# Optimization experiments

Measured on AMD Instinct MI355X. Metric: run time of the kernel, lower is better.

The kernel has to match this reference:

```python
import jax, jax.numpy as jnp
import numpy as np

V, D, H, B, T = 32000, 256, 512, 32, 64


def setup_inputs() -> dict:
    key = jax.random.key(0)
    ks = jax.random.split(key, 8)
    return {
        "word_indices": jax.random.randint(ks[0], (B, T), 0, V),
        "num_words": jax.random.randint(ks[1], (B,), 1, T + 1),
        "encoder_state": jax.random.normal(ks[2], (B, H), jnp.float32),
        # learned params
        "embW": jax.random.uniform(ks[3], (V, D), jnp.float32, -1.0, 1.0),
        "Wg": jax.random.normal(ks[4], (D + H, 2 * H), jnp.float32) * 0.05,  # reset+update gates
        "bg": jnp.ones((2 * H,), jnp.float32),  # TF GRUCell gate bias init = 1.0
        "Wc": jax.random.normal(ks[5], (D + H, H), jnp.float32) * 0.05,      # candidate
        "bc": jnp.zeros((H,), jnp.float32),
        "Wout": jax.random.normal(ks[6], (H, V), jnp.float32) * 0.05,        # Dense(V)
        "bout": jnp.zeros((V,), jnp.float32),
    }


def reference(word_indices, num_words, encoder_state, embW, Wg, bg, Wc, bc, Wout, bout):
    # Embedding lookup: [B, T, D] -> time-major [T, B, D]
    xs = jnp.swapaxes(embW[word_indices], 0, 1)
    # sequence-length mask like tf.nn.static_rnn: [T, B, 1]
    mask = (jnp.arange(T)[:, None] < num_words[None, :])[..., None].astype(xs.dtype)

    def step(h, inp):
        x_t, m_t = inp  # [B, D], [B, 1]
        xh = jnp.concatenate([x_t, h], axis=-1)          # [B, D+H]
        r, u = jnp.split(jax.nn.sigmoid(xh @ Wg + bg), 2, axis=-1)
        c = jnp.tanh(jnp.concatenate([x_t, r * h], axis=-1) @ Wc + bc)
        h_new = u * h + (1.0 - u) * c
        out = h_new * m_t                                 # zero outputs past seq length
        h_next = m_t * h_new + (1.0 - m_t) * h            # carry state past seq length
        return h_next, out

    _, outs = jax.lax.scan(step, encoder_state, (xs, mask))  # outs: [T, B, H]
    logits = jnp.einsum('tbh,hv->btv', outs, Wout) + bout    # [B, T, V]
    return logits
```

## Files before the change

kernel.cpp:

```cpp
#include <hip/hip_runtime.h>
#include <hip/hip_bf16.h>

#define V_ 32000
#define D_ 256
#define H_ 512
#define B_ 32
#define T_ 64
#define NSL 8

typedef __attribute__((ext_vector_type(8))) __bf16 bf16x8;
typedef __attribute__((ext_vector_type(4))) float f32x4;
typedef _Float16 f16x2 __attribute__((ext_vector_type(2)));
typedef unsigned int u32t;
typedef unsigned short u16t;
typedef unsigned long long u64t;

__device__ __forceinline__ u32t pack_h16(float a, float b) {
  union { _Float16 h; unsigned short u; } lo, hi;
  lo.h = (_Float16)a; hi.h = (_Float16)b;
  return (u32t)lo.u | ((u32t)hi.u << 16);
}

__device__ __forceinline__ float f16u_to_f(u16t u) {
  union { _Float16 h; unsigned short u; } x;
  x.u = u;
  return (float)x.h;
}

__device__ __forceinline__ float dot2(u32t w, u32t h, float acc) {
#if __has_builtin(__builtin_amdgcn_fdot2)
  return __builtin_amdgcn_fdot2(__builtin_bit_cast(f16x2, w),
                                __builtin_bit_cast(f16x2, h), acc, false);
#else
  f16x2 a = __builtin_bit_cast(f16x2, w);
  f16x2 b = __builtin_bit_cast(f16x2, h);
  return acc + (float)a.x * (float)b.x + (float)a.y * (float)b.y;
#endif
}

__device__ __forceinline__ void gld_lds16(const void* g, void* l) {
  __builtin_amdgcn_global_load_lds((const __attribute__((address_space(1))) void*)g,
                                   (__attribute__((address_space(3))) void*)l,
                                   16, 0, 0);
}

__device__ __forceinline__ u32t ld_rlx(const u32t* p) {
  return __hip_atomic_load(p, __ATOMIC_RELAXED, __HIP_MEMORY_SCOPE_AGENT);
}
__device__ __forceinline__ void st_rlx(u32t* p, u32t v) {
  __hip_atomic_store(p, v, __ATOMIC_RELAXED, __HIP_MEMORY_SCOPE_AGENT);
}

__global__ __launch_bounds__(256) void k_setup(const float* __restrict__ Wout,
                                               __hip_bfloat16* __restrict__ WoutT,
                                               const float* __restrict__ Wg,
                                               const float* __restrict__ Wc,
                                               const float* __restrict__ enc,
                                               uint4* __restrict__ Wg2,
                                               uint4* __restrict__ Wc2,
                                               u32t* __restrict__ HBT,
                                               u32t* __restrict__ RHT,
                                               const int* __restrict__ widx,
                                               const float* __restrict__ embW,
                                               const float* __restrict__ bg,
                                               const float* __restrict__ bc,
                                               float* __restrict__ pre_g,
                                               float* __restrict__ pre_c) {
  int blk = blockIdx.x;
  int tid = threadIdx.x;

  if (blk < 4000) {
    __shared__ float tile[64][65];
    int v0 = (blk % 500) * 64;
    int h0 = (blk / 500) * 64;
#pragma unroll
    for (int i = 0; i < 16; ++i) {
      int idx = i * 256 + tid;
      int r = idx >> 6;
      int c = idx & 63;
      tile[r][c] = Wout[(size_t)(h0 + r) * V_ + v0 + c];
    }
    __syncthreads();
#pragma unroll
    for (int i = 0; i < 16; ++i) {
      int idx = i * 256 + tid;
      int rv = idx >> 6;
      int ch = idx & 63;
      WoutT[(size_t)(v0 + rv) * H_ + h0 + ch] = __float2bfloat16(tile[ch][rv]);
    }
  } else if (blk < 4448) {
    int pblk = blk - 4000;
    if (pblk < 256) {
      int gid = pblk * 256 + tid;
      int ks = gid & 3;
      int cq = (gid >> 2) & 127;
      int it = (gid >> 9) & 15;
      int s = gid >> 13;
      int j = (cq < 64) ? (s * 64 + cq) : (512 + s * 64 + (cq - 64));
      int k0 = ks * 128 + it * 8;
      uint4 v;
      v.x = pack_h16(Wg[(size_t)(256 + k0 + 0) * 1024 + j], Wg[(size_t)(256 + k0 + 1) * 1024 + j]);
      v.y = pack_h16(Wg[(size_t)(256 + k0 + 2) * 1024 + j], Wg[(size_t)(256 + k0 + 3) * 1024 + j]);
      v.z = pack_h16(Wg[(size_t)(256 + k0 + 4) * 1024 + j], Wg[(size_t)(256 + k0 + 5) * 1024 + j]);
      v.w = pack_h16(Wg[(size_t)(256 + k0 + 6) * 1024 + j], Wg[(size_t)(256 + k0 + 7) * 1024 + j]);
      Wg2[gid] = v;
    } else if (pblk < 384) {
      int gid = (pblk - 256) * 256 + tid;
      int ks8 = gid & 7;
      int cq2 = (gid >> 3) & 63;
      int it = (gid >> 9) & 7;
      int s = gid >> 12;
      int jc = s * 64 + cq2;
      int k0 = ks8 * 64 + it * 8;
      uint4 v;
      v.x = pack_h16(Wc[(size_t)(256 + k0 + 0) * 512 + jc], Wc[(size_t)(256 + k0 + 1) * 512 + jc]);
      v.y = pack_h16(Wc[(size_t)(256 + k0 + 2) * 512 + jc], Wc[(size_t)(256 + k0 + 3) * 512 + jc]);
      v.z = pack_h16(Wc[(size_t)(256 + k0 + 4) * 512 + jc], Wc[(size_t)(256 + k0 + 5) * 512 + jc]);
      v.w = pack_h16(Wc[(size_t)(256 + k0 + 6) * 512 + jc], Wc[(size_t)(256 + k0 + 7) * 512 + jc]);
      Wc2[gid] = v;
    } else {
      int gid = (pblk - 384) * 256 + tid;
      int b = gid >> 9, k = gid & 511;
      u32t hv = pack_h16(enc[b * H_ + k], 0.f) & 0xffffu;
      st_rlx(&HBT[gid], hv);
      st_rlx(&RHT[gid], 0xFFFF0000u);
    }
  } else {
    __shared__ __align__(16) float x2[D_][8];
    __shared__ int wid[8];
    int idx = blk - 4448;
    int bx = idx & 255;
    int by = idx >> 8;
    int n0 = bx * 8;
    if (tid < 8) wid[tid] = widx[n0 + tid];
    __syncthreads();
#pragma unroll
    for (int i = 0; i < 8; ++i)
      x2[tid][i] = embW[(size_t)wid[i] * D_ + tid];
    __syncthreads();

    float acc[8];
    if (by < 4) {
      int J = by * 256 + tid;
      float bias = bg[J];
#pragma unroll
      for (int i = 0; i < 8; ++i) acc[i] = bias;
      for (int d = 0; d < D_; ++d) {
        float4 xa = *(const float4*)&x2[d][0];
        float4 xb = *(const float4*)&x2[d][4];
        float w = Wg[(size_t)d * 1024 + J];
        acc[0] = fmaf(xa.x, w, acc[0]); acc[1] = fmaf(xa.y, w, acc[1]);
        acc[2] = fmaf(xa.z, w, acc[2]); acc[3] = fmaf(xa.w, w, acc[3]);
        acc[4] = fmaf(xb.x, w, acc[4]); acc[5] = fmaf(xb.y, w, acc[5]);
        acc[6] = fmaf(xb.z, w, acc[6]); acc[7] = fmaf(xb.w, w, acc[7]);
      }
#pragma unroll
      for (int i = 0; i < 8; ++i)
        pre_g[(size_t)(n0 + i) * 1024 + J] = acc[i];
    } else {
      int Jc = (by - 4) * 256 + tid;
      float bias = bc[Jc];
#pragma unroll
      for (int i = 0; i < 8; ++i) acc[i] = bias;
      for (int d = 0; d < D_; ++d) {
        float4 xa = *(const float4*)&x2[d][0];
        float4 xb = *(const float4*)&x2[d][4];
        float w = Wc[(size_t)d * 512 + Jc];
        acc[0] = fmaf(xa.x, w, acc[0]); acc[1] = fmaf(xa.y, w, acc[1]);
        acc[2] = fmaf(xa.z, w, acc[2]); acc[3] = fmaf(xa.w, w, acc[3]);
        acc[4] = fmaf(xb.x, w, acc[4]); acc[5] = fmaf(xb.y, w, acc[5]);
        acc[6] = fmaf(xb.z, w, acc[6]); acc[7] = fmaf(xb.w, w, acc[7]);
      }
#pragma unroll
      for (int i = 0; i < 8; ++i)
        pre_c[(size_t)(n0 + i) * 512 + Jc] = acc[i];
    }
  }
}

__global__ __launch_bounds__(512, 2) void k_gru7(const int* __restrict__ num_words,
                                                 const uint4* __restrict__ Wg2,
                                                 const uint4* __restrict__ Wc2,
                                                 const float* __restrict__ pre_g,
                                                 const float* __restrict__ pre_c,
                                                 u32t* __restrict__ RHT,
                                                 u32t* __restrict__ HBT,
                                                 u32t* __restrict__ A32) {
  __shared__ __align__(16) u32t h2_l[256];
  __shared__ __align__(16) u32t rh2_l[256];
  __shared__ float u_l[64];
  int bid = blockIdx.x;
  int b = bid & 31;
  int s = bid >> 5;
  int tid = threadIdx.x;
  int nw = num_words[b];

  int cq = tid >> 2, ks = tid & 3;
  int j1 = (cq < 64) ? (s * 64 + cq) : (512 + s * 64 + (cq - 64));
  int cq2 = tid >> 3, ks8 = tid & 7;
  int jc = s * 64 + cq2;

  uint4 wg[16];
#pragma unroll
  for (int i = 0; i < 16; ++i) {
    int ii = (i + ks) & 15;
    wg[i] = Wg2[(((size_t)s * 16 + ii) * 128 + cq) * 4 + ks];
  }
  uint4 wc[8];
#pragma unroll
  for (int i = 0; i < 8; ++i) {
    int ii = (i + ks8) & 7;
    wc[i] = Wc2[(((size_t)s * 8 + ii) * 64 + cq2) * 8 + ks8];
  }

  u32t* HBp = HBT + (size_t)b * 512;
  u32t* RHp = RHT + (size_t)b * 512;
  bool pub1 = (ks == 0) && (cq < 64);
  bool ulane = (ks == 0) && (cq >= 64);
  bool pub2 = (ks8 == 0);
  bool writer2 = pub2 && ((cq2 & 1) == 0);

  for (int t = 0; t < T_; ++t) {
    float pg = pre_g[((size_t)b * T_ + t) * 1024 + j1];
    float pc = pre_c[((size_t)b * T_ + t) * 512 + jc];

    __syncthreads();
    {
      u32t want = (u32t)t << 16;
      u32t v;
      do { v = ld_rlx(&HBp[tid]); } while ((v & 0xffff0000u) != want);
      ((volatile u16t*)h2_l)[tid] = (u16t)v;
    }
    __syncthreads();

    float a0 = 0.f, a1 = 0.f, a2s = 0.f, a3 = 0.f;
    const uint4* h4 = (const uint4*)h2_l;
#pragma unroll
    for (int i = 0; i < 16; ++i) {
      int ii = (i + ks) & 15;
      uint4 hv = h4[ks * 16 + ii];
      a0 = dot2(wg[i].x, hv.x, a0);
      a1 = dot2(wg[i].y, hv.y, a1);
      a2s = dot2(wg[i].z, hv.z, a2s);
      a3 = dot2(wg[i].w, hv.w, a3);
    }
    float a = (a0 + a1) + (a2s + a3);
    a += __shfl_xor(a, 1);
    a += __shfl_xor(a, 2);
    float gate = 1.f / (1.f + __expf(-(a + pg)));
    if (cq < 64) {
      float hh = f16u_to_f(((const u16t*)h2_l)[s * 64 + cq]);
      if (pub1)
        st_rlx(&RHp[s * 64 + cq],
               (pack_h16(gate * hh, 0.f) & 0xffffu) | ((u32t)(t + 1) << 16));
    } else if (ulane) {
      u_l[cq - 64] = gate;
    }

    {
      u32t want = (u32t)(t + 1) << 16;
      u32t v;
      do { v = ld_rlx(&RHp[tid]); } while ((v & 0xffff0000u) != want);
      ((volatile u16t*)rh2_l)[tid] = (u16t)v;
    }
    __syncthreads();

    float c0 = 0.f, c1 = 0.f, c2 = 0.f, c3 = 0.f;
    const uint4* r4 = (const uint4*)rh2_l;
#pragma unroll
    for (int i = 0; i < 8; ++i) {
      int ii = (i + ks8) & 7;
      uint4 rv = r4[ks8 * 8 + ii];
      c0 = dot2(wc[i].x, rv.x, c0);
      c1 = dot2(wc[i].y, rv.y, c1);
      c2 = dot2(wc[i].z, rv.z, c2);
      c3 = dot2(wc[i].w, rv.w, c3);
    }
    float a2 = (c0 + c1) + (c2 + c3);
    a2 += __shfl_xor(a2, 1);
    a2 += __shfl_xor(a2, 2);
    a2 += __shfl_xor(a2, 4);
    float cv = tanhf(a2 + pc);
    float uu = u_l[cq2];
    float hold = f16u_to_f(((const u16t*)h2_l)[jc]);
    float hn = uu * hold + (1.f - uu) * cv;
    bool live = t < nw;
    float hnext = live ? hn : hold;
    if (pub2)
      st_rlx(&HBp[s * 64 + cq2],
             (pack_h16(hnext, 0.f) & 0xffffu) | ((u32t)(t + 1) << 16));
    u32t ma = (u32t)__hip_bfloat16_raw(__float2bfloat16(live ? hn : 0.f)).x;
    u32t oa = (u32t)__shfl_xor((int)ma, 8);
    if (writer2)
      A32[(((size_t)b * T_ + t) * 512 + jc) >> 1] = ma | (oa << 16);
  }
}

__global__ __launch_bounds__(256) void k_proj(const __hip_bfloat16* __restrict__ Ap,
                                              const __hip_bfloat16* __restrict__ BTp,
                                              const float* __restrict__ bout,
                                              float* __restrict__ C) {
  __shared__ char As[128 * 64 * 2];
  __shared__ char Bs[128 * 64 * 2];
  int tid = threadIdx.x;
  int lane = tid & 63;
  int wave = tid >> 6;
  int m0 = blockIdx.x * 128;
  int n0 = blockIdx.y * 128;
  int wm = wave >> 1, wn = wave & 1;
  f32x4 acc[4][4] = {};

  const char* Ab = (const char*)Ap;
  const char* Bb = (const char*)BTp;

  for (int ks = 0; ks < 8; ++ks) {
    int k0 = ks * 64;
    __syncthreads();
#pragma unroll
    for (int inst = 0; inst < 4; ++inst) {
      int o = inst * 4096 + wave * 1024;
      int ol = o + lane * 16;
      int r = ol >> 7;
      int cb = ol & 127;
      gld_lds16(Ab + ((size_t)(m0 + r) * 512 + k0) * 2 + cb, As + o);
      gld_lds16(Bb + ((size_t)(n0 + r) * 512 + k0) * 2 + cb, Bs + o);
    }
    __syncthreads();
#pragma unroll
    for (int kk = 0; kk < 64; kk += 32) {
      bf16x8 af[4], bfr[4];
      int cbyte = kk * 2 + ((lane >> 4) << 4);
#pragma unroll
      for (int mi = 0; mi < 4; ++mi) {
        int row = wm * 64 + mi * 16 + (lane & 15);
        af[mi] = *(const bf16x8*)(As + row * 128 + cbyte);
      }
#pragma unroll
      for (int ni = 0; ni < 4; ++ni) {
        int row = wn * 64 + ni * 16 + (lane & 15);
        bfr[ni] = *(const bf16x8*)(Bs + row * 128 + cbyte);
      }
#pragma unroll
      for (int mi = 0; mi < 4; ++mi)
#pragma unroll
        for (int ni = 0; ni < 4; ++ni)
          acc[mi][ni] = __builtin_amdgcn_mfma_f32_16x16x32_bf16(bfr[ni], af[mi], acc[mi][ni], 0, 0, 0);
    }
  }
#pragma unroll
  for (int ni = 0; ni < 4; ++ni) {
    int colbase = n0 + wn * 64 + ni * 16 + ((lane >> 4) << 2);
    float4 bb = *(const float4*)&bout[colbase];
#pragma unroll
    for (int mi = 0; mi < 4; ++mi) {
      int row = m0 + wm * 64 + mi * 16 + (lane & 15);
      f32x4 v;
      v.x = acc[mi][ni][0] + bb.x;
      v.y = acc[mi][ni][1] + bb.y;
      v.z = acc[mi][ni][2] + bb.z;
      v.w = acc[mi][ni][3] + bb.w;
      __builtin_nontemporal_store(v, (f32x4*)&C[(size_t)row * V_ + colbase]);
    }
  }
}

extern "C" void kernel_launch(void* const* d_in, const int* in_sizes, int n_in,
                              void* d_out, int out_size, void* d_ws, size_t ws_size,
                              hipStream_t stream) {
  const int* widx = (const int*)d_in[0];
  const int* num_words = (const int*)d_in[1];
  const float* enc = (const float*)d_in[2];
  const float* embW = (const float*)d_in[3];
  const float* Wg = (const float*)d_in[4];
  const float* bg = (const float*)d_in[5];
  const float* Wc = (const float*)d_in[6];
  const float* bc = (const float*)d_in[7];
  const float* Wout = (const float*)d_in[8];
  const float* bout = (const float*)d_in[9];
  float* out = (float*)d_out;

  char* ws = (char*)d_ws;
  float* pre_g = (float*)(ws);
  float* pre_c = (float*)(ws + 8388608);
  __hip_bfloat16* A = (__hip_bfloat16*)(ws + 12582912);
  __hip_bfloat16* WoutT = (__hip_bfloat16*)(ws + 14680064);
  uint4* Wg2 = (uint4*)(ws + 47448064);
  uint4* Wc2 = (uint4*)(ws + 48496640);
  u32t* RHT = (u32t*)(ws + 49020928);
  u32t* HBT = (u32t*)(ws + 49086464);

  hipLaunchKernelGGL(k_setup, dim3(5984), dim3(256), 0, stream,
                     Wout, WoutT, Wg, Wc, enc, Wg2, Wc2, HBT, RHT,
                     widx, embW, bg, bc, pre_g, pre_c);
  hipLaunchKernelGGL(k_gru7, dim3(32 * NSL), dim3(512), 0, stream,
                     num_words, Wg2, Wc2, pre_g, pre_c, RHT, HBT, (u32t*)A);
  hipLaunchKernelGGL(k_proj, dim3(16, 250), dim3(256), 0, stream, A, WoutT, bout, out);
}
```

Baseline: 383.7 us.

## Rewrite output projection GEMM with 256x256 tiles, LDS double-buffering and swizzle

Replaces the 128x128 single-buffered projection GEMM with a 512-thread, 256x256-tile kernel. It double-buffers the LDS K tiles and issues the next tile's global-to-LDS loads while the current tile's MFMAs run. It also XOR-swizzles LDS addresses to cut bank conflicts and raises wave priority around the MFMA bursts. This is meant to hide load latency and raise data reuse per block, but each thread now holds 32 accumulators, which increases register pressure and limits occupancy to one block.

```diff
diff --git a/kernel.cpp b/kernel.cpp
--- a/kernel.cpp
+++ b/kernel.cpp
@@ -296,69 +296,100 @@
   }
 }
 
-__global__ __launch_bounds__(256) void k_proj(const __hip_bfloat16* __restrict__ Ap,
-                                              const __hip_bfloat16* __restrict__ BTp,
-                                              const float* __restrict__ bout,
-                                              float* __restrict__ C) {
-  __shared__ char As[128 * 64 * 2];
-  __shared__ char Bs[128 * 64 * 2];
+__global__ __launch_bounds__(512, 1) void k_proj8(const __hip_bfloat16* __restrict__ Ap,
+                                                  const __hip_bfloat16* __restrict__ BTp,
+                                                  const float* __restrict__ bout,
+                                                  float* __restrict__ C) {
+  __shared__ __align__(16) char LDS[2][2][32768];
   int tid = threadIdx.x;
   int lane = tid & 63;
   int wave = tid >> 6;
-  int m0 = blockIdx.x * 128;
-  int n0 = blockIdx.y * 128;
-  int wm = wave >> 1, wn = wave & 1;
-  f32x4 acc[4][4] = {};
-
+  int wm = wave >> 2;
+  int wn = wave & 3;
+  int m0 = blockIdx.x * 256;
+  int n0 = blockIdx.y * 256;
   const char* Ab = (const char*)Ap;
   const char* Bb = (const char*)BTp;
 
-  for (int ks = 0; ks < 8; ++ks) {
-    int k0 = ks * 64;
-    __syncthreads();
-#pragma unroll
-    for (int inst = 0; inst < 4; ++inst) {
-      int o = inst * 4096 + wave * 1024;
-      int ol = o + lane * 16;
-      int r = ol >> 7;
-      int cb = ol & 127;
-      gld_lds16(Ab + ((size_t)(m0 + r) * 512 + k0) * 2 + cb, As + o);
-      gld_lds16(Bb + ((size_t)(n0 + r) * 512 + k0) * 2 + cb, Bs + o);
-    }
-    __syncthreads();
-#pragma unroll
-    for (int kk = 0; kk < 64; kk += 32) {
-      bf16x8 af[4], bfr[4];
-      int cbyte = kk * 2 + ((lane >> 4) << 4);
-#pragma unroll
-      for (int mi = 0; mi < 4; ++mi) {
-        int row = wm * 64 + mi * 16 + (lane & 15);
-        af[mi] = *(const bf16x8*)(As + row * 128 + cbyte);
+  f32x4 acc[8][4] = {};
+
+  auto STAGE = [&](int d, int op, int kt) {
+    const char* base = op ? Bb : Ab;
+    int r0 = op ? n0 : m0;
+#pragma unroll
+    for (int j = 0; j < 4; ++j) {
+      int o = j * 8192 + wave * 1024;
+      int q = o + lane * 16;
+      int qp = q ^ (((q >> 9) & 1) << 5) ^ (((q >> 10) & 1) << 4);
+      int row = qp >> 7;
+      int scol = qp & 127;
+      gld_lds16(base + ((size_t)(r0 + row) * 512 + kt * 64) * 2 + scol,
+                &LDS[d][op][o]);
+    }
+  };
+
+  STAGE(0, 0, 0);
+  STAGE(0, 1, 0);
+  asm volatile("s_waitcnt vmcnt(0)" ::: "memory");
+  __builtin_amdgcn_s_barrier();
+
+#pragma unroll 1
+  for (int t = 0; t < 8; ++t) {
+    int d = t & 1;
+    char* Abuf = &LDS[d][0][0];
+    char* Bbuf = &LDS[d][1][0];
+#pragma unroll
+    for (int ph = 0; ph < 4; ++ph) {
+      int qr = ph >> 1, qc = ph & 1;
+      int cb0 = (lane >> 4) << 4;
+      bf16x8 af[4][2], bfr[2][2];
+#pragma unroll
+      for (int kk = 0; kk < 2; ++kk) {
+#pragma unroll
+        for (int mi = 0; mi < 4; ++mi) {
+          int row = wm * 128 + qr * 64 + mi * 16 + (lane & 15);
+          int p = row * 128 + kk * 64 + cb0;
+          p = p ^ (((p >> 9) & 1) << 5) ^ (((p >> 10) & 1) << 4);
+          af[mi][kk] = *(const bf16x8*)&Abuf[p];
+        }
+#pragma unroll
+        for (int ni = 0; ni < 2; ++ni) {
+          int row = wn * 64 + qc * 32 + ni * 16 + (lane & 15);
+          int p = row * 128 + kk * 64 + cb0;
+          p = p ^ (((p >> 9) & 1) << 5) ^ (((p >> 10) & 1) << 4);
+          bfr[ni][kk] = *(const bf16x8*)&Bbuf[p];
+        }
       }
-#pragma unroll
-      for (int ni = 0; ni < 4; ++ni) {
-        int row = wn * 64 + ni * 16 + (lane & 15);
-        bfr[ni] = *(const bf16x8*)(Bs + row * 128 + cbyte);
-      }
-#pragma unroll
-      for (int mi = 0; mi < 4; ++mi)
-#pragma unroll
-        for (int ni = 0; ni < 4; ++ni)
-          acc[mi][ni] = __builtin_amdgcn_mfma_f32_16x16x32_bf16(bfr[ni], af[mi], acc[mi][ni], 0, 0, 0);
-    }
-  }
-#pragma unroll
-  for (int ni = 0; ni < 4; ++ni) {
-    int colbase = n0 + wn * 64 + ni * 16 + ((lane >> 4) << 2);
+      if (ph < 2 && t < 7) STAGE(d ^ 1, ph, t + 1);
+      __builtin_amdgcn_s_setprio(1);
+#pragma unroll
+      for (int kk = 0; kk < 2; ++kk)
+#pragma unroll
+        for (int mi = 0; mi < 4; ++mi)
+#pragma unroll
+          for (int ni = 0; ni < 2; ++ni)
+            acc[qr * 4 + mi][qc * 2 + ni] =
+                __builtin_amdgcn_mfma_f32_16x16x32_bf16(bfr[ni][kk], af[mi][kk],
+                                                        acc[qr * 4 + mi][qc * 2 + ni],
+                                                        0, 0, 0);
+      __builtin_amdgcn_s_setprio(0);
+      if (ph == 3) asm volatile("s_waitcnt vmcnt(0)" ::: "memory");
+      __builtin_amdgcn_s_barrier();
+    }
+  }
+
+#pragma unroll
+  for (int fc = 0; fc < 4; ++fc) {
+    int colbase = n0 + wn * 64 + fc * 16 + ((lane >> 4) << 2);
     float4 bb = *(const float4*)&bout[colbase];
 #pragma unroll
-    for (int mi = 0; mi < 4; ++mi) {
-      int row = m0 + wm * 64 + mi * 16 + (lane & 15);
+    for (int fr = 0; fr < 8; ++fr) {
+      int row = m0 + wm * 128 + fr * 16 + (lane & 15);
       f32x4 v;
-      v.x = acc[mi][ni][0] + bb.x;
-      v.y = acc[mi][ni][1] + bb.y;
-      v.z = acc[mi][ni][2] + bb.z;
-      v.w = acc[mi][ni][3] + bb.w;
+      v.x = acc[fr][fc][0] + bb.x;
+      v.y = acc[fr][fc][1] + bb.y;
+      v.z = acc[fr][fc][2] + bb.z;
+      v.w = acc[fr][fc][3] + bb.w;
       __builtin_nontemporal_store(v, (f32x4*)&C[(size_t)row * V_ + colbase]);
     }
   }
@@ -394,5 +425,5 @@
                      widx, embW, bg, bc, pre_g, pre_c);
   hipLaunchKernelGGL(k_gru7, dim3(32 * NSL), dim3(512), 0, stream,
                      num_words, Wg2, Wc2, pre_g, pre_c, RHT, HBT, (u32t*)A);
-  hipLaunchKernelGGL(k_proj, dim3(16, 250), dim3(256), 0, stream, A, WoutT, bout, out);
-}
+  hipLaunchKernelGGL(k_proj8, dim3(8, 125), dim3(512), 0, stream, A, WoutT, bout, out);
+}
```

Measured after the change: 417.1 us. 8.7% more time.
